# Kernel optimization log

Measured on AMD Instinct MI355X. Metric: run time of the kernel, lower is better.

The kernel has to match this reference:

```python
import jax, jax.numpy as jnp
import numpy as np

TEMPERATURE = 0.5
EPS = 1e-8  # torch.nn.CosineSimilarity eps


def setup_inputs() -> dict:
    key = jax.random.key(0)
    k1, k2 = jax.random.split(key)
    B, D = 4096, 128
    z_i = jax.random.normal(k1, (B, D), dtype=jnp.float32)
    z_j = jax.random.normal(k2, (B, D), dtype=jnp.float32)
    return {"z_i": z_i, "z_j": z_j}


def _nt_xent(z_i, z_j, temperature=TEMPERATURE):
    B = z_i.shape[0]
    reps = jnp.concatenate([z_i, z_j], axis=0)                 # [N, D], N = 2B
    norms = jnp.maximum(jnp.linalg.norm(reps, axis=1, keepdims=True), EPS)
    zn = reps / norms                                          # normalize once
    sim = jnp.matmul(zn, zn.T) / temperature                   # [N, N] via GEMM
    exp_sim = jnp.exp(sim)
    # positives: offset-diagonals +B and -B
    idx = jnp.arange(B)
    sim_i_j = exp_sim[idx, idx + B]
    sim_j_i = exp_sim[idx + B, idx]
    pos_pairs = jnp.concatenate([sim_i_j, sim_j_i], axis=0)    # [N]
    sim_self = jnp.diagonal(exp_sim)                           # [N]
    denominator = jnp.sum(exp_sim, axis=1) - sim_self          # [N]
    itemized_loss = -jnp.log(pos_pairs / denominator)
    return jnp.mean(itemized_loss)


def reference(z_i, z_j):
    return _nt_xent(z_i, z_j)
```

## Files before the change

kernel.cpp:

```cpp
#include <hip/hip_runtime.h>
#include <hip/hip_bf16.h>

#define B_ROWS 4096
#define N_ROWS 8192
#define D 128
#define INV_T 2.0f

#define RB 128
#define CS_COLS 1024
#define CHUNK 64
#define LDS_STRIDE 136

typedef __attribute__((ext_vector_type(8))) short bf16x8;
typedef __attribute__((ext_vector_type(4))) float f32x4;

__device__ inline unsigned short f32_to_bf16_rne(float f) {
    unsigned int u = __float_as_uint(f);
    u += 0x7fffu + ((u >> 16) & 1u);
    return (unsigned short)(u >> 16);
}
__device__ inline float bf16s_to_f32(short s) {
    unsigned int u = ((unsigned int)(unsigned short)s) << 16;
    return __uint_as_float(u);
}

__global__ void k_normalize(const float* __restrict__ z_i,
                            const float* __restrict__ z_j,
                            unsigned short* __restrict__ zn) {
    int row  = blockIdx.x;
    int lane = threadIdx.x;
    const float* src = (row < B_ROWS) ? (z_i + (size_t)row * D)
                                      : (z_j + (size_t)(row - B_ROWS) * D);
    float2 v = ((const float2*)src)[lane];
    float ss = v.x * v.x + v.y * v.y;
    #pragma unroll
    for (int m = 1; m < 64; m <<= 1) ss += __shfl_xor(ss, m);
    float rinv = 1.0f / fmaxf(sqrtf(ss), 1e-8f);
    ushort2 o;
    o.x = f32_to_bf16_rne(v.x * rinv);
    o.y = f32_to_bf16_rne(v.y * rinv);
    ((ushort2*)(zn + (size_t)row * D))[lane] = o;
}

__global__ __launch_bounds__(256)
void k_simsum(const unsigned short* __restrict__ zn,
              float* __restrict__ denom) {
    __shared__ unsigned short sB[CHUNK * LDS_STRIDE];
    const int tid  = threadIdx.x;
    const int wave = tid >> 6;
    const int lane = tid & 63;
    const int l15  = lane & 15;
    const int quad = lane >> 4;
    const int m0   = blockIdx.x * RB + wave * 32;

    bf16x8 A[2][4];
    #pragma unroll
    for (int rt = 0; rt < 2; ++rt)
        #pragma unroll
        for (int kb = 0; kb < 4; ++kb)
            A[rt][kb] = *(const bf16x8*)(zn + (size_t)(m0 + rt * 16 + l15) * D + kb * 32 + quad * 8);

    float rs[2][4] = {{0.f,0.f,0.f,0.f},{0.f,0.f,0.f,0.f}};
    const int c_base = blockIdx.y * CS_COLS;

    for (int cb = 0; cb < CS_COLS / CHUNK; ++cb) {
        __syncthreads();
        const int c0 = c_base + cb * CHUNK;
        #pragma unroll
        for (int p = 0; p < 4; ++p) {
            int i  = tid + p * 256;
            int r  = i >> 4;
            int cc = i & 15;
            *(bf16x8*)(sB + r * LDS_STRIDE + cc * 8) =
                *(const bf16x8*)(zn + (size_t)(c0 + r) * D + cc * 8);
        }
        __syncthreads();

        #pragma unroll
        for (int t = 0; t < 4; ++t) {
            bf16x8 b[4];
            #pragma unroll
            for (int kb = 0; kb < 4; ++kb)
                b[kb] = *(const bf16x8*)(sB + (t * 16 + l15) * LDS_STRIDE + kb * 32 + quad * 8);
            f32x4 acc0 = {0.f,0.f,0.f,0.f};
            f32x4 acc1 = {0.f,0.f,0.f,0.f};
            #pragma unroll
            for (int kb = 0; kb < 4; ++kb) {
                acc0 = __builtin_amdgcn_mfma_f32_16x16x32_bf16(A[0][kb], b[kb], acc0, 0, 0, 0);
                acc1 = __builtin_amdgcn_mfma_f32_16x16x32_bf16(A[1][kb], b[kb], acc1, 0, 0, 0);
            }
            #pragma unroll
            for (int j = 0; j < 4; ++j) {
                rs[0][j] += __expf(acc0[j] * INV_T);
                rs[1][j] += __expf(acc1[j] * INV_T);
            }
        }
    }

    #pragma unroll
    for (int rt = 0; rt < 2; ++rt)
        #pragma unroll
        for (int j = 0; j < 4; ++j) {
            float v = rs[rt][j];
            v += __shfl_xor(v, 1);
            v += __shfl_xor(v, 2);
            v += __shfl_xor(v, 4);
            v += __shfl_xor(v, 8);
            rs[rt][j] = v;
        }
    if (l15 == 0) {
        #pragma unroll
        for (int rt = 0; rt < 2; ++rt)
            #pragma unroll
            for (int j = 0; j < 4; ++j)
                atomicAdd(&denom[m0 + rt * 16 + quad * 4 + j], rs[rt][j]);
    }
}

__global__ void k_finalize(const unsigned short* __restrict__ zn,
                           const float* __restrict__ denom,
                           float* __restrict__ out) {
    int i = blockIdx.x * blockDim.x + threadIdx.x;
    int p = (i + B_ROWS) & (N_ROWS - 1);
    const unsigned short* zi = zn + (size_t)i * D;
    const unsigned short* zp = zn + (size_t)p * D;
    float self_dot = 0.f, pos_dot = 0.f;
    #pragma unroll
    for (int c = 0; c < D / 8; ++c) {
        bf16x8 a = *(const bf16x8*)(zi + c * 8);
        bf16x8 b = *(const bf16x8*)(zp + c * 8);
        #pragma unroll
        for (int j = 0; j < 8; ++j) {
            float av = bf16s_to_f32(a[j]);
            float bv = bf16s_to_f32(b[j]);
            self_dot += av * av;
            pos_dot  += av * bv;
        }
    }
    float dnm  = denom[i] - __expf(self_dot * INV_T);
    float loss = __logf(dnm) - pos_dot * INV_T;

    float v = loss;
    #pragma unroll
    for (int m = 1; m < 64; m <<= 1) v += __shfl_xor(v, m);
    __shared__ float ws[4];
    int wave = threadIdx.x >> 6;
    if ((threadIdx.x & 63) == 0) ws[wave] = v;
    __syncthreads();
    if (threadIdx.x == 0) {
        float s = ws[0] + ws[1] + ws[2] + ws[3];
        atomicAdd(out, s * (1.0f / (float)N_ROWS));
    }
}

extern "C" void kernel_launch(void* const* d_in, const int* in_sizes, int n_in,
                              void* d_out, int out_size, void* d_ws, size_t ws_size,
                              hipStream_t stream) {
    const float* z_i = (const float*)d_in[0];
    const float* z_j = (const float*)d_in[1];
    float* out = (float*)d_out;

    unsigned short* zn = (unsigned short*)d_ws;
    float* denom = (float*)((char*)d_ws + (size_t)N_ROWS * D * 2);

    hipMemsetAsync(denom, 0, N_ROWS * sizeof(float), stream);
    hipMemsetAsync(out, 0, sizeof(float), stream);

    k_normalize<<<N_ROWS, 64, 0, stream>>>(z_i, z_j, zn);
    k_simsum<<<dim3(N_ROWS / RB, N_ROWS / CS_COLS), 256, 0, stream>>>(zn, denom);
    k_finalize<<<N_ROWS / 256, 256, 0, stream>>>(zn, denom, out);
}
```

Before: 95.23 us.

## Enlarge row tile, double-buffer swizzled LDS, use native exp2/log2

The similarity kernel now gives each wave 64 rows instead of 32 and splits columns into 512-wide slices. It double-buffers the column chunks in LDS with register prefetch and an XOR swizzle that replaces the padding. exp and log are computed with the native exp2/log2 builtins using prescaled constants, and normalize packs four rows per block. The aim is more MFMA reuse per LDS load, overlap of global loads with compute, and cheaper transcendentals, at the cost of more registers and pressure on occupancy.

Result: slower. 99.24 us (+4.2%).

```diff
diff --git a/kernel.cpp b/kernel.cpp
--- a/kernel.cpp
+++ b/kernel.cpp
@@ -4,12 +4,13 @@
 #define B_ROWS 4096
 #define N_ROWS 8192
 #define D 128
-#define INV_T 2.0f
+#define SCALE 2.885390081777927f
+#define LN2 0.6931471805599453f
 
-#define RB 128
-#define CS_COLS 1024
+#define RB 256
+#define CSPLIT 512
 #define CHUNK 64
-#define LDS_STRIDE 136
+#define NCHUNK (CSPLIT / CHUNK)
 
 typedef __attribute__((ext_vector_type(8))) short bf16x8;
 typedef __attribute__((ext_vector_type(4))) float f32x4;
@@ -27,8 +28,8 @@
 __global__ void k_normalize(const float* __restrict__ z_i,
                             const float* __restrict__ z_j,
                             unsigned short* __restrict__ zn) {
-    int row  = blockIdx.x;
-    int lane = threadIdx.x;
+    int row  = blockIdx.x * 4 + (threadIdx.x >> 6);
+    int lane = threadIdx.x & 63;
     const float* src = (row < B_ROWS) ? (z_i + (size_t)row * D)
                                       : (z_j + (size_t)(row - B_ROWS) * D);
     float2 v = ((const float2*)src)[lane];
@@ -42,63 +43,84 @@
     ((ushort2*)(zn + (size_t)row * D))[lane] = o;
 }
 
-__global__ __launch_bounds__(256)
+__global__ __launch_bounds__(256, 2)
 void k_simsum(const unsigned short* __restrict__ zn,
               float* __restrict__ denom) {
-    __shared__ unsigned short sB[CHUNK * LDS_STRIDE];
+    __shared__ unsigned short sB[2 * CHUNK * 16 * 8];
     const int tid  = threadIdx.x;
     const int wave = tid >> 6;
     const int lane = tid & 63;
     const int l15  = lane & 15;
     const int quad = lane >> 4;
-    const int m0   = blockIdx.x * RB + wave * 32;
+    const int m0   = blockIdx.x * RB + wave * 64;
 
-    bf16x8 A[2][4];
+    bf16x8 A[4][4];
     #pragma unroll
-    for (int rt = 0; rt < 2; ++rt)
+    for (int rt = 0; rt < 4; ++rt)
         #pragma unroll
         for (int kb = 0; kb < 4; ++kb)
             A[rt][kb] = *(const bf16x8*)(zn + (size_t)(m0 + rt * 16 + l15) * D + kb * 32 + quad * 8);
 
-    float rs[2][4] = {{0.f,0.f,0.f,0.f},{0.f,0.f,0.f,0.f}};
-    const int c_base = blockIdx.y * CS_COLS;
+    float rs[4][4];
+    #pragma unroll
+    for (int rt = 0; rt < 4; ++rt)
+        #pragma unroll
+        for (int j = 0; j < 4; ++j) rs[rt][j] = 0.f;
 
-    for (int cb = 0; cb < CS_COLS / CHUNK; ++cb) {
-        __syncthreads();
-        const int c0 = c_base + cb * CHUNK;
+    const int c_base = blockIdx.y * CSPLIT;
+
+    float4 st[4];
+    #pragma unroll
+    for (int p = 0; p < 4; ++p) {
+        int i = tid + p * 256, c = i >> 4, j = i & 15;
+        st[p] = *(const float4*)(zn + (size_t)(c_base + c) * D + j * 8);
+    }
+
+    for (int cb = 0; cb < NCHUNK; ++cb) {
+        unsigned short* buf = sB + (cb & 1) * (CHUNK * 16 * 8);
         #pragma unroll
         for (int p = 0; p < 4; ++p) {
-            int i  = tid + p * 256;
-            int r  = i >> 4;
-            int cc = i & 15;
-            *(bf16x8*)(sB + r * LDS_STRIDE + cc * 8) =
-                *(const bf16x8*)(zn + (size_t)(c0 + r) * D + cc * 8);
+            int i = tid + p * 256, c = i >> 4, j = i & 15;
+            int piece = c * 16 + (j ^ (c & 7));
+            *(float4*)(buf + piece * 8) = st[p];
         }
         __syncthreads();
+
+        if (cb + 1 < NCHUNK) {
+            #pragma unroll
+            for (int p = 0; p < 4; ++p) {
+                int i = tid + p * 256, c = i >> 4, j = i & 15;
+                st[p] = *(const float4*)(zn + (size_t)(c_base + (cb + 1) * CHUNK + c) * D + j * 8);
+            }
+        }
 
         #pragma unroll
         for (int t = 0; t < 4; ++t) {
             bf16x8 b[4];
             #pragma unroll
+            for (int kb = 0; kb < 4; ++kb) {
+                int c = t * 16 + l15;
+                int piece = c * 16 + ((kb * 4 + quad) ^ (c & 7));
+                b[kb] = *(const bf16x8*)(buf + piece * 8);
+            }
+            f32x4 acc[4];
+            #pragma unroll
+            for (int rt = 0; rt < 4; ++rt) acc[rt] = (f32x4){0.f, 0.f, 0.f, 0.f};
+            #pragma unroll
             for (int kb = 0; kb < 4; ++kb)
-                b[kb] = *(const bf16x8*)(sB + (t * 16 + l15) * LDS_STRIDE + kb * 32 + quad * 8);
-            f32x4 acc0 = {0.f,0.f,0.f,0.f};
-            f32x4 acc1 = {0.f,0.f,0.f,0.f};
+                #pragma unroll
+                for (int rt = 0; rt < 4; ++rt)
+                    acc[rt] = __builtin_amdgcn_mfma_f32_16x16x32_bf16(A[rt][kb], b[kb], acc[rt], 0, 0, 0);
             #pragma unroll
-            for (int kb = 0; kb < 4; ++kb) {
-                acc0 = __builtin_amdgcn_mfma_f32_16x16x32_bf16(A[0][kb], b[kb], acc0, 0, 0, 0);
-                acc1 = __builtin_amdgcn_mfma_f32_16x16x32_bf16(A[1][kb], b[kb], acc1, 0, 0, 0);
-            }
-            #pragma unroll
-            for (int j = 0; j < 4; ++j) {
-                rs[0][j] += __expf(acc0[j] * INV_T);
-                rs[1][j] += __expf(acc1[j] * INV_T);
-            }
+            for (int rt = 0; rt < 4; ++rt)
+                #pragma unroll
+                for (int j = 0; j < 4; ++j)
+                    rs[rt][j] += __builtin_amdgcn_exp2f(acc[rt][j] * SCALE);
         }
     }
 
     #pragma unroll
-    for (int rt = 0; rt < 2; ++rt)
+    for (int rt = 0; rt < 4; ++rt)
         #pragma unroll
         for (int j = 0; j < 4; ++j) {
             float v = rs[rt][j];
@@ -110,7 +132,7 @@
         }
     if (l15 == 0) {
         #pragma unroll
-        for (int rt = 0; rt < 2; ++rt)
+        for (int rt = 0; rt < 4; ++rt)
             #pragma unroll
             for (int j = 0; j < 4; ++j)
                 atomicAdd(&denom[m0 + rt * 16 + quad * 4 + j], rs[rt][j]);
@@ -137,8 +159,8 @@
             pos_dot  += av * bv;
         }
     }
-    float dnm  = denom[i] - __expf(self_dot * INV_T);
-    float loss = __logf(dnm) - pos_dot * INV_T;
+    float dnm  = denom[i] - __builtin_amdgcn_exp2f(self_dot * SCALE);
+    float loss = __builtin_amdgcn_logf(dnm) * LN2 - pos_dot * 2.0f;
 
     float v = loss;
     #pragma unroll
@@ -166,7 +188,7 @@
     hipMemsetAsync(denom, 0, N_ROWS * sizeof(float), stream);
     hipMemsetAsync(out, 0, sizeof(float), stream);
 
-    k_normalize<<<N_ROWS, 64, 0, stream>>>(z_i, z_j, zn);
-    k_simsum<<<dim3(N_ROWS / RB, N_ROWS / CS_COLS), 256, 0, stream>>>(zn, denom);
+    k_normalize<<<N_ROWS / 4, 256, 0, stream>>>(z_i, z_j, zn);
+    k_simsum<<<dim3(N_ROWS / RB, N_ROWS / CSPLIT), 256, 0, stream>>>(zn, denom);
     k_finalize<<<N_ROWS / 256, 256, 0, stream>>>(zn, denom, out);
 }
```
